# Performance work log

Hardware: AMD Instinct MI355X
Metric: run time of the kernel (lower is better)

## Reference

```python
import jax, jax.numpy as jnp
import numpy as np
import math

D = 512
H = 512


def setup_inputs() -> dict:
    key = jax.random.key(0)
    k1, k2, k3, k4 = jax.random.split(key, 4)
    x = jax.random.normal(k1, (32, 2048, D), dtype=jnp.float32)
    h0 = jax.random.normal(k2, (32, H), dtype=jnp.float32)
    Wx = jax.random.normal(k3, (D, 4 * H), dtype=jnp.float32) / math.sqrt(D)
    Wh = jax.random.normal(k4, (H, 4 * H), dtype=jnp.float32) / math.sqrt(H)
    b = jnp.zeros((4 * H,), dtype=jnp.float32)
    return {"x": x, "h0": h0, "Wx": Wx, "Wh": Wh, "b": b}


def lstm_forward(x, h0, Wx, Wh, b):
    # Precompute input projection for all timesteps: (N,T,4H)
    affine_x = jnp.einsum('ntd,dk->ntk', x, Wx) + b
    c0 = jnp.zeros_like(h0)
    Hdim = h0.shape[1]

    def step(carry, ax_t):
        h, c = carry
        affine = ax_t + h @ Wh  # (N,4H)
        i, f, o, g = jnp.split(affine, 4, axis=1)
        i = jax.nn.sigmoid(i)
        f = jax.nn.sigmoid(f)
        o = jax.nn.sigmoid(o)
        g = jnp.tanh(g)
        c_next = f * c + i * g
        h_next = o * jnp.tanh(c_next)
        return (h_next, c_next), h_next

    # scan over time: move T to leading axis
    (_, _), hs = jax.lax.scan(step, (h0, c0), jnp.swapaxes(affine_x, 0, 1))
    return jnp.swapaxes(hs, 0, 1)  # (N,T,H)


def reference(x, h0, Wx, Wh, b):
    return lstm_forward(x, h0, Wx, Wh, b)
```

## Files before the change

### kernel.cpp

```cpp
#include <hip/hip_runtime.h>

typedef __attribute__((ext_vector_type(8))) short short8;
typedef __attribute__((ext_vector_type(8))) unsigned short ushort8;
typedef __attribute__((ext_vector_type(4))) float f32x4;
typedef __attribute__((ext_vector_type(4))) int i32x4;

#define T_STEPS 2048

static __device__ __forceinline__ unsigned short f2bf(float f) {
  unsigned u = __builtin_bit_cast(unsigned, f);
  unsigned r = u + 0x7fffu + ((u >> 16) & 1u);
  return (unsigned short)(r >> 16);
}
static __device__ __forceinline__ float bf2f(unsigned short h) {
  unsigned u = ((unsigned)h) << 16;
  return __builtin_bit_cast(float, u);
}
static __device__ __forceinline__ float fast_sigmoid(float v) {
  return __builtin_amdgcn_rcpf(1.0f + __expf(-v));
}
static __device__ __forceinline__ float fast_tanh(float v) {
  return 1.0f - 2.0f * __builtin_amdgcn_rcpf(1.0f + __expf(2.0f * v));
}

__global__ void prep_kernel(const float* __restrict__ Wx, const float* __restrict__ Wh,
                            const float* __restrict__ h0,
                            unsigned short* __restrict__ wxp, unsigned short* __restrict__ whp,
                            unsigned short* __restrict__ hbuf, int* __restrict__ ctl,
                            int* __restrict__ flags) {
  int idx = blockIdx.x * 256 + threadIdx.x;
  if (idx < 2097152) {
    int which = idx >> 20;
    int r = idx & 1048575;
    int e = r & 7;
    int l = (r >> 3) & 63;
    int kt = (r >> 9) & 15;
    int g = (r >> 13) & 3;
    int s = r >> 15;
    int k = kt * 32 + ((l >> 4) << 3) + e;
    int c = g * 512 + s * 16 + (l & 15);
    const float* W = which ? Wh : Wx;
    unsigned short* dst = which ? whp : wxp;
    dst[r] = f2bf(W[k * 2048 + c]);
  } else if (idx < 2097152 + 16384) {
    int i = idx - 2097152;
    int bg = i >> 9;
    int k = i & 511;
    int g = bg >> 2, bl = bg & 3;
    float v = h0[i];
    unsigned short hi = f2bf(v) & 0xFFFCu;
    unsigned short lo = f2bf(v - bf2f(hi)) & 0xFFFCu;
    unsigned short* d = hbuf + g * 131072;
#pragma unroll
    for (int rep = 0; rep < 4; ++rep) {
      d[rep * 4096 + bl * 512 + k] = hi;
      d[rep * 4096 + 2048 + bl * 512 + k] = lo;
    }
  } else if (idx < 2097152 + 16384 + 9) {
    ctl[idx - (2097152 + 16384)] = 0;
  } else if (idx < 2097152 + 16384 + 9 + 8192) {
    flags[idx - (2097152 + 16384 + 9)] = 0;
  }
}

__global__ void xprep_kernel(const float* __restrict__ x, unsigned short* __restrict__ xb) {
  size_t i8 = ((size_t)blockIdx.x * 256 + threadIdx.x) * 8;
  int t = (int)(i8 >> 14);
  int r = (int)(i8 & 16383);
  int b = r >> 9;
  int d = r & 511;
  const float* src = x + ((size_t)b * 2048 + (size_t)t) * 512 + d;
  f32x4 a = *(const f32x4*)src;
  f32x4 c = *(const f32x4*)(src + 4);
  ushort8 o;
#pragma unroll
  for (int e = 0; e < 4; ++e) {
    o[e] = f2bf(a[e]);
    o[e + 4] = f2bf(c[e]);
  }
  *(ushort8*)(xb + i8) = o;
}

__global__ __launch_bounds__(256, 1) void scan_kernel(
    const unsigned short* __restrict__ xb, const float* __restrict__ bias,
    const unsigned short* __restrict__ wxp, const unsigned short* __restrict__ whp,
    unsigned short* __restrict__ hbuf, float* __restrict__ out, int* __restrict__ ctl,
    int* __restrict__ flags) {
  __shared__ unsigned short WxL[4][16][512];
  __shared__ unsigned short WhL[4][16][512];
  __shared__ float gLDS[2][4][4][4][16];
  __shared__ int s_g, s_s, s_dir;

  const int tid = threadIdx.x;
  const int lane = tid & 63;
  const int gw = tid >> 6;

  if (tid == 0) {
    unsigned xcc;
    asm volatile("s_getreg_b32 %0, hwreg(HW_REG_XCC_ID)" : "=s"(xcc));
    xcc &= 7;
    int tk = __hip_atomic_fetch_add(&ctl[xcc], 1, __ATOMIC_RELAXED,
                                    __HIP_MEMORY_SCOPE_AGENT);
    int c[8];
    for (;;) {
      int tot = 0;
#pragma unroll
      for (int x = 0; x < 8; ++x) {
        c[x] = __hip_atomic_load(&ctl[x], __ATOMIC_RELAXED, __HIP_MEMORY_SCOPE_AGENT);
        tot += c[x];
      }
      if (tot >= 256) break;
      __builtin_amdgcn_s_sleep(2);
    }
    int g = -1, s = -1, dir = 0;
    if (tk < 32) {
      g = (int)xcc;
      s = tk;
      dir = (c[xcc] >= 32);
    } else {
      int rank = __hip_atomic_fetch_add(&ctl[8], 1, __ATOMIC_RELAXED,
                                        __HIP_MEMORY_SCOPE_AGENT);
      int acc2 = 0;
      for (int x = 0; x < 8; ++x) {
        int n = 32 - c[x];
        if (n < 0) n = 0;
        if (g < 0 && rank < acc2 + n) { g = x; s = c[x] + (rank - acc2); }
        acc2 += n;
      }
      dir = 0;
    }
    s_g = g; s_s = s; s_dir = dir;
  }
  __syncthreads();
  const int g = s_g, s = s_s, use_direct = s_dir;
  if (s < 0 || g < 0) return;

  {
    const ushort8* sx = (const ushort8*)(wxp + (size_t)s * 32768);
    const ushort8* sh = (const ushort8*)(whp + (size_t)s * 32768);
    ushort8* dx = (ushort8*)&WxL[0][0][0];
    ushort8* dh = (ushort8*)&WhL[0][0][0];
    for (int i = tid; i < 4096; i += 256) {
      dx[i] = sx[i];
      dh[i] = sh[i];
    }
  }
  __syncthreads();
  short8 wxf[4][4], whf[4][4];
#pragma unroll
  for (int kt = 0; kt < 4; ++kt)
#pragma unroll
    for (int nt = 0; nt < 4; ++nt) {
      const int ktg = (gw << 2) + kt;
      wxf[kt][nt] = *(const short8*)&WxL[nt][ktg][lane * 8];
      whf[kt][nt] = *(const short8*)&WhL[nt][ktg][lane * 8];
    }

  const int brow = lane & 3;
  const int kgrp = (lane >> 4) * 8;
  const int gb = lane >> 4;
  const int gu = lane & 15;
  float bias4[4];
#pragma unroll
  for (int gg2 = 0; gg2 < 4; ++gg2)
    bias4[gg2] = bias[gg2 * 512 + s * 16 + gu];
  float c = 0.f;

  unsigned short* hb = hbuf + g * 131072;
  int* gflags = flags + g * 1024;
  int* wflag = gflags + ((gw << 3) + (lane & 7)) * 32;
  int* myflag = gflags + s * 32;
  float* outbase = out + (size_t)(g * 4 + gb) * (2048 * 512) + s * 16 + gu;
  const int xrow = (g * 4 + brow) * 512;
  const int shfl_src = ((lane >> 3) << 4) + ((lane & 7) << 1);

  short8 xf[4];
#pragma unroll
  for (int kt = 0; kt < 4; ++kt) {
    const int k0 = (gw << 7) + (kt << 5) + kgrp;
    xf[kt] = *(const short8*)&xb[xrow + k0];
  }

  for (int t = 0; t < T_STEPS; ++t) {
    const unsigned tag = (unsigned)((t >> 3) & 3);
    const unsigned tp32 = 0x00010001u * tag;
    const unsigned short* srd = hb + (t & 7) * 16384;
    i32x4 q[8];
    bool ok = false;

    if (use_direct) {
      const unsigned short* hrd = srd + ((unsigned)gw & 3u) * 4096;
#pragma unroll
      for (int kt = 0; kt < 4; ++kt) {
        const int k0 = (gw << 7) + (kt << 5) + kgrp;
        q[kt * 2 + 0] = *(const i32x4*)(hrd + brow * 512 + k0);
        q[kt * 2 + 1] = *(const i32x4*)(hrd + 2048 + brow * 512 + k0);
      }
    }

    f32x4 acc[4], accl[4];
#pragma unroll
    for (int nt = 0; nt < 4; ++nt) {
      acc[nt] = (f32x4){0.f, 0.f, 0.f, 0.f};
      accl[nt] = (f32x4){0.f, 0.f, 0.f, 0.f};
    }
#pragma unroll
    for (int kt = 0; kt < 4; ++kt)
#pragma unroll
      for (int nt = 0; nt < 4; ++nt)
        acc[nt] = __builtin_amdgcn_mfma_f32_16x16x32_bf16(xf[kt], wxf[kt][nt], acc[nt], 0, 0, 0);

    if (use_direct) {
      unsigned bad = 0;
#pragma unroll
      for (int i = 0; i < 8; ++i)
#pragma unroll
        for (int j = 0; j < 4; ++j)
          bad |= (((unsigned)q[i][j]) & 0x00030003u) ^ tp32;
      ok = __all(bad == 0);
      for (int a = 1; a < 24 && !ok; ++a) {
        if (a >= 2) __builtin_amdgcn_s_sleep(2);
        asm volatile("" ::: "memory");
        const unsigned short* hrd = srd + ((unsigned)(a + gw) & 3u) * 4096;
#pragma unroll
        for (int kt = 0; kt < 4; ++kt) {
          const int k0 = (gw << 7) + (kt << 5) + kgrp;
          q[kt * 2 + 0] = *(const i32x4*)(hrd + brow * 512 + k0);
          q[kt * 2 + 1] = *(const i32x4*)(hrd + 2048 + brow * 512 + k0);
        }
        unsigned bad2 = 0;
#pragma unroll
        for (int i = 0; i < 8; ++i)
#pragma unroll
          for (int j = 0; j < 4; ++j)
            bad2 |= (((unsigned)q[i][j]) & 0x00030003u) ^ tp32;
        ok = __all(bad2 == 0);
      }
    }

    if (!ok) {
      if (use_direct && t > 0) {
        int done = (lane >= 8);
        for (;;) {
          if (!done) {
            int old, zero = 0;
            asm volatile("global_atomic_add %0, %1, %2, off sc0\n\t"
                         "s_waitcnt vmcnt(0)"
                         : "=v"(old) : "v"(wflag), "v"(zero) : "memory");
            done = (old >= t);
          }
          if (__all(done)) break;
          __builtin_amdgcn_s_sleep(1);
        }
      }
      const unsigned long long tp64 = 0x0001000100010001ull * (unsigned long long)tag;
      const unsigned long long* h64 = (const unsigned long long*)srd;
      for (;;) {
        unsigned long long bad = 0;
#pragma unroll
        for (int kt = 0; kt < 4; ++kt) {
          const int k0 = (gw << 7) + (kt << 5) + kgrp;
          const int bi = (brow * 512 + k0) >> 2;
          const int bj = (2048 + brow * 512 + k0) >> 2;
          union { unsigned long long u[2]; i32x4 v; } a, b;
          a.u[0] = __hip_atomic_load(h64 + bi, __ATOMIC_RELAXED, __HIP_MEMORY_SCOPE_AGENT);
          a.u[1] = __hip_atomic_load(h64 + bi + 1, __ATOMIC_RELAXED, __HIP_MEMORY_SCOPE_AGENT);
          b.u[0] = __hip_atomic_load(h64 + bj, __ATOMIC_RELAXED, __HIP_MEMORY_SCOPE_AGENT);
          b.u[1] = __hip_atomic_load(h64 + bj + 1, __ATOMIC_RELAXED, __HIP_MEMORY_SCOPE_AGENT);
          q[kt * 2 + 0] = a.v;
          q[kt * 2 + 1] = b.v;
          bad |= (a.u[0] & 0x0003000300030003ull) ^ tp64;
          bad |= (a.u[1] & 0x0003000300030003ull) ^ tp64;
          bad |= (b.u[0] & 0x0003000300030003ull) ^ tp64;
          bad |= (b.u[1] & 0x0003000300030003ull) ^ tp64;
        }
        if (__all(bad == 0)) break;
        __builtin_amdgcn_s_sleep(1);
      }
    }

#pragma unroll
    for (int kt = 0; kt < 4; ++kt) {
      short8 hh = __builtin_bit_cast(short8, q[kt * 2 + 0]);
      short8 hl = __builtin_bit_cast(short8, q[kt * 2 + 1]);
#pragma unroll
      for (int nt = 0; nt < 4; ++nt) {
        acc[nt] = __builtin_amdgcn_mfma_f32_16x16x32_bf16(hh, whf[kt][nt], acc[nt], 0, 0, 0);
        accl[nt] = __builtin_amdgcn_mfma_f32_16x16x32_bf16(hl, whf[kt][nt], accl[nt], 0, 0, 0);
      }
    }

    if (lane < 16) {
#pragma unroll
      for (int nt = 0; nt < 4; ++nt)
#pragma unroll
        for (int r = 0; r < 4; ++r)
          gLDS[t & 1][gw][nt][r][lane] = acc[nt][r] + accl[nt][r];
    }
    __syncthreads();

    float v4[4];
#pragma unroll
    for (int gg2 = 0; gg2 < 4; ++gg2) {
      float sum = bias4[gg2];
#pragma unroll
      for (int w = 0; w < 4; ++w) sum += gLDS[t & 1][w][gg2][gb][gu];
      v4[gg2] = sum;
    }
    float ig = fast_sigmoid(v4[0]);
    float fg = fast_sigmoid(v4[1]);
    float og = fast_sigmoid(v4[2]);
    float gg3 = fast_tanh(v4[3]);
    c = fg * c + ig * gg3;
    float h = og * fast_tanh(c);

    if (gw == 0 && t + 1 < T_STEPS) {
      const unsigned ntag = (unsigned)(((t + 1) >> 3) & 3);
      float ha = __shfl(h, shfl_src);
      float hbv = __shfl(h, shfl_src + 1);
      unsigned short hiA = (unsigned short)((f2bf(ha) & 0xFFFCu) | ntag);
      unsigned short loA = (unsigned short)((f2bf(ha - bf2f(hiA)) & 0xFFFCu) | ntag);
      unsigned short hiB = (unsigned short)((f2bf(hbv) & 0xFFFCu) | ntag);
      unsigned short loB = (unsigned short)((f2bf(hbv - bf2f(hiB)) & 0xFFFCu) | ntag);
      unsigned whi = (unsigned)hiA | ((unsigned)hiB << 16);
      unsigned wlo = (unsigned)loA | ((unsigned)loB << 16);
      if (lane < 32) {
        const int b = lane >> 3, u2 = (lane & 7) * 2;
        unsigned short* wr = hb + ((t + 1) & 7) * 16384;
        if (use_direct) {
#pragma unroll
          for (int rep = 0; rep < 4; ++rep) {
            *(unsigned*)&wr[rep * 4096 + b * 512 + s * 16 + u2] = whi;
            *(unsigned*)&wr[rep * 4096 + 2048 + b * 512 + s * 16 + u2] = wlo;
          }
        } else {
#pragma unroll
          for (int rep = 0; rep < 4; ++rep) {
            __hip_atomic_store((unsigned*)&wr[rep * 4096 + b * 512 + s * 16 + u2], whi,
                               __ATOMIC_RELAXED, __HIP_MEMORY_SCOPE_AGENT);
            __hip_atomic_store((unsigned*)&wr[rep * 4096 + 2048 + b * 512 + s * 16 + u2], wlo,
                               __ATOMIC_RELAXED, __HIP_MEMORY_SCOPE_AGENT);
          }
        }
      }
      asm volatile("s_waitcnt vmcnt(0)" ::: "memory");
      if (lane == 0) {
        int one = 1;
        asm volatile("global_atomic_add %0, %1, off" :: "v"(myflag), "v"(one) : "memory");
      }
    }

    if (gw == 1) outbase[(size_t)t * 512] = h;
    {
      const int tn = (t + 1 < T_STEPS) ? (t + 1) : t;
      const unsigned short* xt1 = xb + (size_t)tn * 16384;
#pragma unroll
      for (int kt = 0; kt < 4; ++kt) {
        const int k0 = (gw << 7) + (kt << 5) + kgrp;
        xf[kt] = *(const short8*)&xt1[xrow + k0];
      }
    }
  }
}

extern "C" void kernel_launch(void* const* d_in, const int* in_sizes, int n_in,
                              void* d_out, int out_size, void* d_ws, size_t ws_size,
                              hipStream_t stream) {
  const float* x = (const float*)d_in[0];
  const float* h0 = (const float*)d_in[1];
  const float* Wx = (const float*)d_in[2];
  const float* Wh = (const float*)d_in[3];
  const float* bias = (const float*)d_in[4];
  float* out = (float*)d_out;

  char* ws = (char*)d_ws;
  unsigned short* wxp = (unsigned short*)(ws);
  unsigned short* whp = (unsigned short*)(ws + (2u << 20));
  unsigned short* hbuf = (unsigned short*)(ws + (4u << 20));
  int* ctl = (int*)(ws + (6u << 20) + (512u << 10));
  int* flags = (int*)(ws + (7u << 20));
  unsigned short* xb = (unsigned short*)(ws + (8u << 20));

  hipLaunchKernelGGL(prep_kernel, dim3(8289), dim3(256), 0, stream,
                     Wx, Wh, h0, wxp, whp, hbuf, ctl, flags);
  hipLaunchKernelGGL(xprep_kernel, dim3(16384), dim3(256), 0, stream, x, xb);
  hipLaunchKernelGGL(scan_kernel, dim3(256), dim3(256), 0, stream,
                     xb, bias, wxp, whp, hbuf, out, ctl, flags);
}
```

Before: 6.777 ms.

## Use 12 hidden-state replicas with 4-slot ring and per-warp replica assignment

Widens the replicated hidden-state broadcast buffer from 4 to 12 copies per slot and shrinks the ring from 8 to 4 time slots, so each warp reads its own replica set (3*gw). The polling retry loop now walks the other replicas without sleeping, instead of retrying up to 24 times with s_sleep. This is meant to spread polling reads across more cache lines and lower cross-block handoff latency per step. In exchange, each producer issues three times as many stores per step, and the shorter ring reuses slots sooner, which changes the tag period and the workspace layout.

New measurement: 6.977 ms. +3.0%, slower.

```diff
diff --git a/kernel.cpp b/kernel.cpp
--- a/kernel.cpp
+++ b/kernel.cpp
@@ -6,6 +6,9 @@
 typedef __attribute__((ext_vector_type(4))) int i32x4;
 
 #define T_STEPS 2048
+#define NREP 12
+#define SLOT_STRIDE (NREP * 4096)
+#define GRP_STRIDE (4 * SLOT_STRIDE)
 
 static __device__ __forceinline__ unsigned short f2bf(float f) {
   unsigned u = __builtin_bit_cast(unsigned, f);
@@ -50,9 +53,8 @@
     float v = h0[i];
     unsigned short hi = f2bf(v) & 0xFFFCu;
     unsigned short lo = f2bf(v - bf2f(hi)) & 0xFFFCu;
-    unsigned short* d = hbuf + g * 131072;
-#pragma unroll
-    for (int rep = 0; rep < 4; ++rep) {
+    unsigned short* d = hbuf + g * GRP_STRIDE;
+    for (int rep = 0; rep < NREP; ++rep) {
       d[rep * 4096 + bl * 512 + k] = hi;
       d[rep * 4096 + 2048 + bl * 512 + k] = lo;
     }
@@ -166,7 +168,7 @@
     bias4[gg2] = bias[gg2 * 512 + s * 16 + gu];
   float c = 0.f;
 
-  unsigned short* hb = hbuf + g * 131072;
+  unsigned short* hb = hbuf + g * GRP_STRIDE;
   int* gflags = flags + g * 1024;
   int* wflag = gflags + ((gw << 3) + (lane & 7)) * 32;
   int* myflag = gflags + s * 32;
@@ -182,14 +184,14 @@
   }
 
   for (int t = 0; t < T_STEPS; ++t) {
-    const unsigned tag = (unsigned)((t >> 3) & 3);
+    const unsigned tag = (unsigned)((t >> 2) & 3);
     const unsigned tp32 = 0x00010001u * tag;
-    const unsigned short* srd = hb + (t & 7) * 16384;
+    const unsigned short* srd = hb + (t & 3) * SLOT_STRIDE;
     i32x4 q[8];
     bool ok = false;
 
     if (use_direct) {
-      const unsigned short* hrd = srd + ((unsigned)gw & 3u) * 4096;
+      const unsigned short* hrd = srd + (unsigned)(3 * gw) * 4096;
 #pragma unroll
       for (int kt = 0; kt < 4; ++kt) {
         const int k0 = (gw << 7) + (kt << 5) + kgrp;
@@ -218,10 +220,11 @@
         for (int j = 0; j < 4; ++j)
           bad |= (((unsigned)q[i][j]) & 0x00030003u) ^ tp32;
       ok = __all(bad == 0);
-      for (int a = 1; a < 24 && !ok; ++a) {
-        if (a >= 2) __builtin_amdgcn_s_sleep(2);
+      for (int a = 1; a < NREP && !ok; ++a) {
         asm volatile("" ::: "memory");
-        const unsigned short* hrd = srd + ((unsigned)(a + gw) & 3u) * 4096;
+        int rep = 3 * gw + a;
+        if (rep >= NREP) rep -= NREP;
+        const unsigned short* hrd = srd + (unsigned)rep * 4096;
 #pragma unroll
         for (int kt = 0; kt < 4; ++kt) {
           const int k0 = (gw << 7) + (kt << 5) + kgrp;
@@ -315,7 +318,7 @@
     float h = og * fast_tanh(c);
 
     if (gw == 0 && t + 1 < T_STEPS) {
-      const unsigned ntag = (unsigned)(((t + 1) >> 3) & 3);
+      const unsigned ntag = (unsigned)(((t + 1) >> 2) & 3);
       float ha = __shfl(h, shfl_src);
       float hbv = __shfl(h, shfl_src + 1);
       unsigned short hiA = (unsigned short)((f2bf(ha) & 0xFFFCu) | ntag);
@@ -326,16 +329,16 @@
       unsigned wlo = (unsigned)loA | ((unsigned)loB << 16);
       if (lane < 32) {
         const int b = lane >> 3, u2 = (lane & 7) * 2;
-        unsigned short* wr = hb + ((t + 1) & 7) * 16384;
+        unsigned short* wr = hb + ((t + 1) & 3) * SLOT_STRIDE;
         if (use_direct) {
 #pragma unroll
-          for (int rep = 0; rep < 4; ++rep) {
+          for (int rep = 0; rep < NREP; ++rep) {
             *(unsigned*)&wr[rep * 4096 + b * 512 + s * 16 + u2] = whi;
             *(unsigned*)&wr[rep * 4096 + 2048 + b * 512 + s * 16 + u2] = wlo;
           }
         } else {
 #pragma unroll
-          for (int rep = 0; rep < 4; ++rep) {
+          for (int rep = 0; rep < NREP; ++rep) {
             __hip_atomic_store((unsigned*)&wr[rep * 4096 + b * 512 + s * 16 + u2], whi,
                                __ATOMIC_RELAXED, __HIP_MEMORY_SCOPE_AGENT);
             __hip_atomic_store((unsigned*)&wr[rep * 4096 + 2048 + b * 512 + s * 16 + u2], wlo,
@@ -377,8 +380,8 @@
   unsigned short* wxp = (unsigned short*)(ws);
   unsigned short* whp = (unsigned short*)(ws + (2u << 20));
   unsigned short* hbuf = (unsigned short*)(ws + (4u << 20));
-  int* ctl = (int*)(ws + (6u << 20) + (512u << 10));
-  int* flags = (int*)(ws + (7u << 20));
+  int* ctl = (int*)(ws + (7u << 20));
+  int* flags = (int*)(ws + (7u << 20) + (64u << 10));
   unsigned short* xb = (unsigned short*)(ws + (8u << 20));
 
   hipLaunchKernelGGL(prep_kernel, dim3(8289), dim3(256), 0, stream,
```
